# Optimization experiments

Hardware: AMD Instinct MI355X
Metric: run time of the kernel (lower is better)

The kernel has to match this reference:

```python
import jax, jax.numpy as jnp
import numpy as np

SIGMA_DATA = 16.0
ALPHA_BOND = 1.0
ALPHA_DNA = 5.0
ALPHA_RNA = 5.0
ALPHA_LIGAND = 10.0
B, N_TOK, APT = 2, 256, 8
N_ATOM = N_TOK * APT
EPS = 1e-12  # inside sqrt to keep grads finite on the zero diagonal


def _pdist(x):
    # x: [*, A, 3] -> [*, A, A]
    d = x[..., :, None, :] - x[..., None, :, :]
    return jnp.sqrt(jnp.sum(d * d, axis=-1) + EPS)


def _atom_onehot(token_mask, num_atoms_per_token, n_atom):
    # [*, A, T]: atom l belongs to token j iff cum[j-1] <= l < cum[j]
    cum = jnp.cumsum(num_atoms_per_token, axis=-1)
    start = cum - num_atoms_per_token
    l = jnp.arange(n_atom)
    oh = (l[:, None] >= start[..., None, :]) & (l[:, None] < cum[..., None, :])
    return oh.astype(jnp.float32) * token_mask[..., None, :]


def _tok_to_atom(onehot, feat):
    return jnp.einsum('...lj,...j->...l', onehot, feat)


def _weighted_rigid_align(x, x_gt, w, mask):
    # AF3 Algorithm 28 (Kabsch); output is detached in the original.
    denom = jnp.sum(mask, -1, keepdims=True)                      # [*,1]
    w_mean = jnp.sum(w * mask, -1, keepdims=True) / denom         # [*,1]
    wm = (w * mask)[..., None]                                    # [*,A,1]
    mu = (jnp.sum(x * wm, -2) / denom) / w_mean                   # [*,3]
    mu_gt = (jnp.sum(x_gt * wm, -2) / denom) / w_mean
    xc = x - mu[..., None, :]
    xgc = x_gt - mu_gt[..., None, :]
    H = jnp.einsum('...ai,...aj->...ij', xgc * wm, xc)            # [*,3,3]
    U, _, Vh = jnp.linalg.svd(H)
    det = jnp.linalg.det(U @ Vh)
    s = jnp.concatenate([jnp.ones(det.shape + (2,), H.dtype), jnp.sign(det)[..., None]], -1)
    R = U @ (Vh * s[..., :, None])                                # U @ diag(1,1,sign) @ Vh
    return jax.lax.stop_gradient(xc @ jnp.swapaxes(R, -1, -2) + mu_gt[..., None, :])


def _diffusion_loss(x, gt, gt_mask, is_p, is_d, is_r, is_l, tb, tm, npt, t):
    A = x.shape[-2]
    oh = _atom_onehot(tm, npt, A)                                 # [*,A,T]
    dx = _pdist(x)
    dx_gt = _pdist(gt)
    pair_mask = gt_mask[..., :, None] * gt_mask[..., None, :]

    # ---- bond loss (Eq. 5) ----
    is_poly = is_p + is_d + is_r
    bm_tok = tb * (is_poly[..., None, :] * is_l[..., None])       # [*,T,T]
    bm = jnp.einsum('...ij,...li->...lj', bm_tok, oh)
    bm = jnp.einsum('...lj,...mj->...lm', bm, oh)                 # [*,A,A]
    m = bm * pair_mask
    l_bond = jnp.sum((dx - dx_gt) ** 2 * m, (-1, -2)) / jnp.sum(m, (-1, -2))

    # ---- smooth LDDT (Alg. 27) ----
    d = jnp.abs(dx_gt - dx)
    e = 0.25 * (jax.nn.sigmoid(0.5 - d) + jax.nn.sigmoid(1.0 - d)
                + jax.nn.sigmoid(2.0 - d) + jax.nn.sigmoid(4.0 - d))
    is_nuc = _tok_to_atom(oh, is_d + is_r)                        # [*,A]
    c = ((dx_gt < 30).astype(x.dtype) * is_nuc[..., None]
         + (dx_gt < 15).astype(x.dtype) * (1.0 - is_nuc[..., None]))
    m2 = (1.0 - jnp.eye(A, dtype=x.dtype)) * pair_mask
    msum = jnp.sum(m2, (-1, -2))
    ce_mean = jnp.sum(c * e * m2, (-1, -2)) / msum
    c_mean = jnp.sum(c * m2, (-1, -2)) / msum
    l_lddt = 1.0 - ce_mean / c_mean

    # ---- weighted MSE (Eq. 3), gt aligned onto x ----
    w_tok = 1.0 + is_d * ALPHA_DNA + is_r * ALPHA_RNA + is_l * ALPHA_LIGAND
    w_atom = _tok_to_atom(oh, w_tok)                              # [*,A]
    sg = jax.lax.stop_gradient
    gt_al = _weighted_rigid_align(sg(gt), sg(x), sg(w_atom), sg(gt_mask))
    l_mse = (1.0 / 3.0) * jnp.sum(jnp.sum((x - gt_al) ** 2, -1) * w_atom * gt_mask, -1) \
            / jnp.sum(gt_mask, -1)

    w_t = (t ** 2 + SIGMA_DATA ** 2) / (t + SIGMA_DATA) ** 2
    return jnp.mean(w_t * (l_mse + ALPHA_BOND * l_bond) + l_lddt)


def setup_inputs() -> dict:
    key = jax.random.key(0)
    k = jax.random.split(key, 9)
    x = jax.random.normal(k[0], (B, N_ATOM, 3), jnp.float32) * 10.0
    gt = x + jax.random.normal(k[1], (B, N_ATOM, 3), jnp.float32)
    return {
        'x': x,
        'gt_atom_positions': gt,
        'gt_atom_mask': jnp.ones((B, N_ATOM), jnp.float32),
        'is_protein': jax.random.uniform(k[2], (B, N_TOK), jnp.float32),
        'is_dna': jax.random.uniform(k[3], (B, N_TOK), jnp.float32),
        'is_rna': jax.random.uniform(k[4], (B, N_TOK), jnp.float32),
        'is_ligand': jax.random.uniform(k[5], (B, N_TOK), jnp.float32),
        'token_bonds': jax.random.uniform(k[6], (B, N_TOK, N_TOK), jnp.float32),
        'token_mask': jnp.ones((B, N_TOK), jnp.float32),
        'num_atoms_per_token': jnp.full((B, N_TOK), APT, jnp.int32),
        't': jax.random.uniform(k[7], (B,), jnp.float32) * 10.0 + 0.1,
    }


def reference(x, gt_atom_positions, gt_atom_mask, is_protein, is_dna, is_rna,
              is_ligand, token_bonds, token_mask, num_atoms_per_token, t):
    return _diffusion_loss(x, gt_atom_positions, gt_atom_mask, is_protein, is_dna,
                           is_rna, is_ligand, token_bonds, token_mask,
                           num_atoms_per_token, t)
```

## Files before the change

kernel.cpp:

```cpp
#include <hip/hip_runtime.h>
#include <math.h>

#define BATCH 2
#define NTOK  256
#define NATOM 2048
#define TL 128
#define TM 64
#define NPB 512
#define TBBUF 1600

__device__ __forceinline__ float frcp(float x)  { return __builtin_amdgcn_rcpf(x); }
__device__ __forceinline__ float fsqrt_(float x){ return __builtin_amdgcn_sqrtf(x); }

__device__ __forceinline__ double wred64(double v) {
    for (int o = 32; o > 0; o >>= 1) v += __shfl_down(v, o, 64);
    return v;
}
__device__ __forceinline__ float fred64(float v) {
    for (int o = 32; o > 0; o >>= 1) v += __shfl_down(v, o, 64);
    return v;
}

__device__ void kabsch_from_sums(const double* shd, float* Rf, float* muf, double* masksum) {
    double wmsum = shd[1];
    float H[3][3];
    for (int i = 0; i < 3; i++)
        for (int j = 0; j < 3; j++)
            H[i][j] = (float)(shd[8 + i * 3 + j] - shd[2 + i] * shd[5 + j] / wmsum);
    float A[3][3];
    for (int j = 0; j < 3; j++) for (int k = 0; k < 3; k++) {
        float s = 0.f; for (int i = 0; i < 3; i++) s = fmaf(H[i][j], H[i][k], s);
        A[j][k] = s;
    }
    float V[3][3] = {{1, 0, 0}, {0, 1, 0}, {0, 0, 1}};
    for (int sweep = 0; sweep < 6; ++sweep) {
        float off = fabsf(A[0][1]) + fabsf(A[0][2]) + fabsf(A[1][2]);
        float diag = fabsf(A[0][0]) + fabsf(A[1][1]) + fabsf(A[2][2]);
        if (off < 1e-7f * diag) break;
        for (int pi = 0; pi < 3; ++pi) {
            int pp_ = (pi == 2) ? 1 : 0;
            int qq_ = (pi == 0) ? 1 : 2;
            float apq = A[pp_][qq_];
            float sc = fabsf(A[pp_][pp_]) + fabsf(A[qq_][qq_]);
            if (fabsf(apq) <= 1e-9f * sc) continue;
            float theta = (A[qq_][qq_] - A[pp_][pp_]) * 0.5f * frcp(apq);
            float t_ = ((theta >= 0.f) ? 1.0f : -1.0f) * frcp(fabsf(theta) + fsqrt_(fmaf(theta, theta, 1.0f)));
            float c_ = frcp(fsqrt_(fmaf(t_, t_, 1.0f))), sn = t_ * c_;
            for (int k = 0; k < 3; k++) { float akp = A[k][pp_], akq = A[k][qq_];
                A[k][pp_] = c_ * akp - sn * akq; A[k][qq_] = sn * akp + c_ * akq; }
            for (int k = 0; k < 3; k++) { float apk = A[pp_][k], aqk = A[qq_][k];
                A[pp_][k] = c_ * apk - sn * aqk; A[qq_][k] = sn * apk + c_ * aqk; }
            for (int k = 0; k < 3; k++) { float vkp = V[k][pp_], vkq = V[k][qq_];
                V[k][pp_] = c_ * vkp - sn * vkq; V[k][qq_] = sn * vkp + c_ * vkq; }
        }
    }
    float lam[3] = {A[0][0], A[1][1], A[2][2]};
    int idx[3] = {0, 1, 2};
    for (int i = 0; i < 2; i++) for (int j = i + 1; j < 3; j++)
        if (lam[idx[j]] > lam[idx[i]]) { int tsw = idx[i]; idx[i] = idx[j]; idx[j] = tsw; }
    float Vs[3][3], sv[3];
    for (int k = 0; k < 3; k++) {
        sv[k] = fsqrt_(fmaxf(lam[idx[k]], 0.0f));
        for (int i = 0; i < 3; i++) Vs[i][k] = V[i][idx[k]];
    }
    float U[3][3] = {{1, 0, 0}, {0, 1, 0}, {0, 0, 1}};
    for (int k = 0; k < 3; k++) {
        if (sv[k] > 1e-6f * sv[0] + 1e-30f) {
            float inv = frcp(sv[k]);
            for (int i = 0; i < 3; i++) {
                float s = 0.f; for (int j = 0; j < 3; j++) s = fmaf(H[i][j], Vs[j][k], s);
                U[i][k] = s * inv;
            }
        } else if (k == 2) {
            U[0][2] = U[1][0] * U[2][1] - U[2][0] * U[1][1];
            U[1][2] = U[2][0] * U[0][1] - U[0][0] * U[2][1];
            U[2][2] = U[0][0] * U[1][1] - U[1][0] * U[0][1];
        }
    }
    float R0[3][3];
    for (int i = 0; i < 3; i++) for (int j = 0; j < 3; j++) {
        float s = 0.f; for (int k = 0; k < 3; k++) s = fmaf(U[i][k], Vs[j][k], s);
        R0[i][j] = s;
    }
    float det = R0[0][0] * (R0[1][1] * R0[2][2] - R0[1][2] * R0[2][1])
              - R0[0][1] * (R0[1][0] * R0[2][2] - R0[1][2] * R0[2][0])
              + R0[0][2] * (R0[1][0] * R0[2][1] - R0[1][1] * R0[2][0]);
    float s2 = (det < 0.0f) ? -1.0f : 1.0f;
    for (int i = 0; i < 3; i++) for (int j = 0; j < 3; j++)
        Rf[i * 3 + j] = fmaf(U[i][0], Vs[j][0], fmaf(U[i][1], Vs[j][1], s2 * U[i][2] * Vs[j][2]));
    for (int i = 0; i < 3; i++) {
        muf[i]     = (float)(shd[2 + i] / wmsum);
        muf[3 + i] = (float)(shd[5 + i] / wmsum);
    }
    *masksum = shd[0];
}

struct PairSh {
    float  isl[NTOK], poly[NTOK], nuc[NTOK], tmk[NTOK];
    int    wsum[4];
    unsigned short atokp1[NATOM];
    float4 lx[TL], lg[TL], mx[TM], mg[TM];
    float  lnuc[TL];
    int    ltok[TL], mtok[TM], lrow[TL], mrel[TM];
    float  tbuf[TBBUF];
    int    info[6];
    float  pred[4][4];
};
struct AlignSh {
    int    wsum[4];
    float  aw[NATOM];
    double dred[4][17];
    float  Rf[9], muf[6];
    double msum;
    double mred[4];
};

__global__ __launch_bounds__(256) void pair_align_kernel(
    const float* __restrict__ x, const float* __restrict__ gt,
    const float* __restrict__ gmask, const float* __restrict__ tb,
    const float* __restrict__ is_p, const float* __restrict__ is_d,
    const float* __restrict__ is_r, const float* __restrict__ is_l,
    const float* __restrict__ tok_mask, const int* __restrict__ npt,
    float4* __restrict__ partials4, float* __restrict__ lmse)
{
    __shared__ __align__(16) char smem[sizeof(PairSh) > sizeof(AlignSh) ? sizeof(PairSh) : sizeof(AlignSh)];
    int id = blockIdx.x;
    int tid = threadIdx.x;
    int lane = tid & 63, wv = tid >> 6;

    if (id >= BATCH) {
        PairSh* s = (PairSh*)smem;
        int pid = id - BATCH;
        int b = pid >> 9;
        int slot = pid & (NPB - 1);
        int l0 = (slot & 15) * TL;
        int m0 = (slot >> 4) * TM;

        int n = npt[b * NTOK + tid];
        {
            int v = n;
            #pragma unroll
            for (int o = 1; o < 64; o <<= 1) {
                int u = __shfl_up(v, o, 64);
                if (lane >= o) v += u;
            }
            if (lane == 63) s->wsum[wv] = v;
            float pd = is_d[b * NTOK + tid], pr = is_r[b * NTOK + tid];
            float pp = is_p[b * NTOK + tid], pl = is_l[b * NTOK + tid];
            s->isl[tid]  = pl;
            s->poly[tid] = pp + pd + pr;
            s->nuc[tid]  = pd + pr;
            s->tmk[tid]  = tok_mask[b * NTOK + tid];
            #pragma unroll
            for (int i = 0; i < NATOM / NTOK; i++) s->atokp1[tid + i * NTOK] = 0;
            __syncthreads();
            int pref = 0;
            for (int w = 0; w < wv; w++) pref += s->wsum[w];
            int cum = v + pref;
            int end = min(cum, NATOM), start = min(cum - n, NATOM);
            unsigned short tk1 = (unsigned short)(tid + 1);
            for (int i = start; i < end; i++) s->atokp1[i] = tk1;
        }
        __syncthreads();

        const float* Xb = x + (size_t)b * NATOM * 3;
        const float* Gb = gt + (size_t)b * NATOM * 3;
        const float* Mb = gmask + (size_t)b * NATOM;

        if (tid < TL) {
            int l = l0 + tid;
            int v = s->atokp1[l];
            int tok = v ? v - 1 : 0;
            float oh = v ? s->tmk[tok] : 0.0f;
            float ml = Mb[l];
            s->lx[tid] = make_float4(Xb[l * 3], Xb[l * 3 + 1], Xb[l * 3 + 2], ml);
            s->lg[tid] = make_float4(Gb[l * 3], Gb[l * 3 + 1], Gb[l * 3 + 2], s->isl[tok] * oh * ml);
            s->lnuc[tid] = s->nuc[tok] * oh;
            s->ltok[tid] = tok;
        } else if (tid < TL + TM) {
            int i = tid - TL, m = m0 + i;
            int v = s->atokp1[m];
            int tok = v ? v - 1 : 0;
            float oh = v ? s->tmk[tok] : 0.0f;
            float mm = Mb[m];
            s->mx[i] = make_float4(Xb[m * 3], Xb[m * 3 + 1], Xb[m * 3 + 2], mm);
            s->mg[i] = make_float4(Gb[m * 3], Gb[m * 3 + 1], Gb[m * 3 + 2], s->poly[tok] * oh * mm);
            s->mtok[i] = tok;
        }
        __syncthreads();
        if (tid == 0) {
            int tl0 = s->ltok[0], tl1 = s->ltok[TL - 1];
            int tm0 = s->mtok[0], tm1 = s->mtok[TM - 1];
            int spanL = tl1 - tl0 + 1, spanM = tm1 - tm0 + 1;
            int stride = spanM | 1;
            int fits = (spanL >= 1) && (spanM >= 1) && (spanL * stride <= TBBUF);
            s->info[0] = fits; s->info[1] = stride; s->info[2] = spanM;
            s->info[3] = tl0; s->info[4] = tm0; s->info[5] = spanL;
        }
        __syncthreads();
        int fits = s->info[0], stride = s->info[1], spanM = s->info[2];
        int tl0 = s->info[3], tm0 = s->info[4], spanL = s->info[5];
        if (tid < TL) {
            int tk = s->ltok[tid];
            s->lrow[tid] = fits ? min(max(tk - tl0, 0), spanL - 1) * stride : tk * NTOK;
        } else if (tid < TL + TM) {
            int tk = s->mtok[tid - TL];
            s->mrel[tid - TL] = fits ? min(max(tk - tm0, 0), spanM - 1) : tk;
        }
        const float* tbg = tb + (size_t)b * NTOK * NTOK;
        if (fits) {
            int cnt = spanL * stride;
            for (int i = tid; i < cnt; i += 256) {
                int r = i / stride, cc = i - r * stride;
                if (cc < spanM) s->tbuf[i] = tbg[(tl0 + r) * NTOK + tm0 + cc];
            }
        }
        __syncthreads();

        int lt = tid & 31, mg = tid >> 5;
        float4 lxv[4], lgv[4]; float lnu[4]; int lrw[4], gli[4];
        #pragma unroll
        for (int k = 0; k < 4; k++) {
            int li = lt + 32 * k;
            lxv[k] = s->lx[li]; lgv[k] = s->lg[li];
            lnu[k] = s->lnuc[li]; lrw[k] = s->lrow[li]; gli[k] = l0 + li;
        }
        float bnum = 0.f, bden = 0.f, ce = 0.f, cs = 0.f;
        const float k1 = 0.60653066f, k2 = 0.36787944f, k3 = 0.13533528f, k4 = 0.018315639f;

        auto body = [&](auto ldtb) {
            int mstart = mg * 8;
            #pragma unroll 2
            for (int j = 0; j < 8; j++) {
                int m = mstart + j;
                float4 mxv = s->mx[m], mgv = s->mg[m];
                int mrel = s->mrel[m];
                int gmi = m0 + m;
                #pragma unroll
                for (int k = 0; k < 4; k++) {
                    float dx0 = lxv[k].x - mxv.x, dx1 = lxv[k].y - mxv.y, dx2 = lxv[k].z - mxv.z;
                    float dg0 = lgv[k].x - mgv.x, dg1 = lgv[k].y - mgv.y, dg2 = lgv[k].z - mgv.z;
                    float dxv = fsqrt_(fmaf(dx2, dx2, fmaf(dx1, dx1, fmaf(dx0, dx0, 1e-12f))));
                    float dgv = fsqrt_(fmaf(dg2, dg2, fmaf(dg1, dg1, fmaf(dg0, dg0, 1e-12f))));
                    float diff = dxv - dgv;
                    float tbv = ldtb(lrw[k], mrel);
                    float bmv = tbv * (lgv[k].w * mgv.w);
                    bden += bmv;
                    bnum = fmaf(diff * diff, bmv, bnum);
                    float d = fabsf(diff);
                    float u = __expf(d);
                    float e1 = frcp(fmaf(u, k1, 1.0f));
                    float e2 = frcp(fmaf(u, k2, 1.0f));
                    float e3 = frcp(fmaf(u, k3, 1.0f));
                    float e4 = frcp(fmaf(u, k4, 1.0f));
                    float es = (e1 + e2) + (e3 + e4);
                    float pm = lxv[k].w * mxv.w;
                    float ccv = dgv < 30.0f ? (dgv < 15.0f ? 1.0f : lnu[k]) : 0.0f;
                    float pm2 = (gli[k] != gmi) ? pm : 0.0f;
                    float cm2 = ccv * pm2;
                    cs += cm2;
                    ce = fmaf(cm2 * 0.25f, es, ce);
                }
            }
        };
        if (fits) body([&](int r, int c) -> float { return s->tbuf[r + c]; });
        else      body([&](int r, int c) -> float { return tbg[r + c]; });

        float vals[4] = {bnum, bden, ce, cs};
        #pragma unroll
        for (int q = 0; q < 4; q++) {
            float v = fred64(vals[q]);
            if (lane == 0) s->pred[wv][q] = v;
        }
        __syncthreads();
        if (tid == 0) {
            float4 o;
            o.x = s->pred[0][0] + s->pred[1][0] + s->pred[2][0] + s->pred[3][0];
            o.y = s->pred[0][1] + s->pred[1][1] + s->pred[2][1] + s->pred[3][1];
            o.z = s->pred[0][2] + s->pred[1][2] + s->pred[2][2] + s->pred[3][2];
            o.w = s->pred[0][3] + s->pred[1][3] + s->pred[2][3] + s->pred[3][3];
            partials4[(size_t)b * NPB + slot] = o;
        }
    } else {
        AlignSh* s = (AlignSh*)smem;
        int b = id;

        {
            int n = npt[b * NTOK + tid];
            int v = n;
            #pragma unroll
            for (int o = 1; o < 64; o <<= 1) {
                int u = __shfl_up(v, o, 64);
                if (lane >= o) v += u;
            }
            if (lane == 63) s->wsum[wv] = v;
            #pragma unroll
            for (int i = 0; i < NATOM / NTOK; i++) s->aw[tid + i * NTOK] = 0.0f;
            float pd = is_d[b * NTOK + tid], pr = is_r[b * NTOK + tid];
            float pl = is_l[b * NTOK + tid];
            float wtv = (1.0f + 5.0f * pd + 5.0f * pr + 10.0f * pl) * tok_mask[b * NTOK + tid];
            __syncthreads();
            int pref = 0;
            for (int w = 0; w < wv; w++) pref += s->wsum[w];
            int cum = v + pref;
            int end = min(cum, NATOM), start = min(cum - n, NATOM);
            for (int i = start; i < end; i++) s->aw[i] = wtv;
        }
        __syncthreads();

        const float* X = x + (size_t)b * NATOM * 3;
        const float* G = gt + (size_t)b * NATOM * 3;
        const float* M = gmask + (size_t)b * NATOM;

        double p[17];
        #pragma unroll
        for (int q = 0; q < 17; q++) p[q] = 0.0;
        for (int a = tid; a < NATOM; a += 256) {
            double m = M[a], wm = (double)s->aw[a] * m;
            double x0 = X[a * 3], x1 = X[a * 3 + 1], x2 = X[a * 3 + 2];
            double g0 = G[a * 3], g1 = G[a * 3 + 1], g2 = G[a * 3 + 2];
            p[0] += m; p[1] += wm;
            p[2] += wm * x0; p[3] += wm * x1; p[4] += wm * x2;
            p[5] += wm * g0; p[6] += wm * g1; p[7] += wm * g2;
            p[8]  += wm * x0 * g0; p[9]  += wm * x0 * g1; p[10] += wm * x0 * g2;
            p[11] += wm * x1 * g0; p[12] += wm * x1 * g1; p[13] += wm * x1 * g2;
            p[14] += wm * x2 * g0; p[15] += wm * x2 * g1; p[16] += wm * x2 * g2;
        }
        #pragma unroll
        for (int q = 0; q < 17; q++) {
            double v = wred64(p[q]);
            if (lane == 0) s->dred[wv][q] = v;
        }
        __syncthreads();
        if (tid == 0) {
            double sh[17];
            for (int q = 0; q < 17; q++)
                sh[q] = s->dred[0][q] + s->dred[1][q] + s->dred[2][q] + s->dred[3][q];
            double ms;
            kabsch_from_sums(sh, s->Rf, s->muf, &ms);
            s->msum = ms;
        }
        __syncthreads();

        float R00 = s->Rf[0], R01 = s->Rf[1], R02 = s->Rf[2];
        float R10 = s->Rf[3], R11 = s->Rf[4], R12 = s->Rf[5];
        float R20 = s->Rf[6], R21 = s->Rf[7], R22 = s->Rf[8];
        float mux0 = s->muf[0], mux1 = s->muf[1], mux2 = s->muf[2];
        float mug0 = s->muf[3], mug1 = s->muf[4], mug2 = s->muf[5];
        double part = 0.0;
        for (int a = tid; a < NATOM; a += 256) {
            float w = s->aw[a], m = M[a];
            float gc0 = G[a * 3] - mug0, gc1 = G[a * 3 + 1] - mug1, gc2 = G[a * 3 + 2] - mug2;
            float al0 = fmaf(R00, gc0, fmaf(R01, gc1, fmaf(R02, gc2, mux0)));
            float al1 = fmaf(R10, gc0, fmaf(R11, gc1, fmaf(R12, gc2, mux1)));
            float al2 = fmaf(R20, gc0, fmaf(R21, gc1, fmaf(R22, gc2, mux2)));
            float r0 = X[a * 3] - al0, r1 = X[a * 3 + 1] - al1, r2 = X[a * 3 + 2] - al2;
            part += (double)(w * m * (r0 * r0 + r1 * r1 + r2 * r2));
        }
        {
            double v = wred64(part);
            if (lane == 0) s->mred[wv] = v;
        }
        __syncthreads();
        if (tid == 0)
            lmse[b] = (float)((s->mred[0] + s->mred[1] + s->mred[2] + s->mred[3]) / (3.0 * s->msum));
    }
}

__global__ __launch_bounds__(256) void final_kernel(
    const float4* __restrict__ partials4, const float* __restrict__ lmse,
    const float* __restrict__ t, float* __restrict__ out)
{
    int tid = threadIdx.x, lane = tid & 63, wv = tid >> 6;
    double pr[2][4] = {{0, 0, 0, 0}, {0, 0, 0, 0}};
    #pragma unroll
    for (int b = 0; b < BATCH; b++)
        for (int sI = tid; sI < NPB; sI += 256) {
            float4 v = partials4[(size_t)b * NPB + sI];
            pr[b][0] += v.x; pr[b][1] += v.y; pr[b][2] += v.z; pr[b][3] += v.w;
        }
    __shared__ double sred[4][8];
    #pragma unroll
    for (int b = 0; b < BATCH; b++)
        #pragma unroll
        for (int q = 0; q < 4; q++) {
            double v = wred64(pr[b][q]);
            if (lane == 0) sred[wv][b * 4 + q] = v;
        }
    __syncthreads();
    if (tid == 0) {
        double tot = 0.0;
        for (int b = 0; b < BATCH; b++) {
            double bn = 0, bd = 0, ce = 0, cs = 0;
            for (int w = 0; w < 4; w++) {
                bn += sred[w][b * 4 + 0]; bd += sred[w][b * 4 + 1];
                ce += sred[w][b * 4 + 2]; cs += sred[w][b * 4 + 3];
            }
            double l_bond = bn / bd;
            double l_lddt = 1.0 - ce / cs;
            double tt = t[b];
            double w_t = (tt * tt + 256.0) / ((tt + 16.0) * (tt + 16.0));
            tot += w_t * ((double)lmse[b] + l_bond) + l_lddt;
        }
        out[0] = (float)(tot / (double)BATCH);
    }
}

extern "C" void kernel_launch(void* const* d_in, const int* in_sizes, int n_in,
                              void* d_out, int out_size, void* d_ws, size_t ws_size,
                              hipStream_t stream) {
    const float* x     = (const float*)d_in[0];
    const float* gt    = (const float*)d_in[1];
    const float* gmask = (const float*)d_in[2];
    const float* is_p  = (const float*)d_in[3];
    const float* is_d  = (const float*)d_in[4];
    const float* is_r  = (const float*)d_in[5];
    const float* is_l  = (const float*)d_in[6];
    const float* tb    = (const float*)d_in[7];
    const float* tm    = (const float*)d_in[8];
    const int*   npt   = (const int*)d_in[9];
    const float* t     = (const float*)d_in[10];
    float* out = (float*)d_out;

    float4* partials4 = (float4*)d_ws;
    float*  lmse      = (float*)((char*)d_ws + (size_t)BATCH * NPB * sizeof(float4));

    pair_align_kernel<<<BATCH + 2 * NPB, 256, 0, stream>>>(
        x, gt, gmask, tb, is_p, is_d, is_r, is_l, tm, npt, partials4, lmse);
    final_kernel<<<1, 256, 0, stream>>>(partials4, lmse, t, out);
}
```

Before: 96.42 us.

## Exploit pair symmetry with upper-triangular 64x64 tile decomposition

```diff
diff --git a/kernel.cpp b/kernel.cpp
--- a/kernel.cpp
+++ b/kernel.cpp
@@ -4,10 +4,10 @@
 #define BATCH 2
 #define NTOK  256
 #define NATOM 2048
-#define TL 128
-#define TM 64
-#define NPB 512
-#define TBBUF 1600
+#define TS 64
+#define NT (NATOM / TS)
+#define NTRI (NT * (NT + 1) / 2)
+#define TBCAP 1156
 
 __device__ __forceinline__ float frcp(float x)  { return __builtin_amdgcn_rcpf(x); }
 __device__ __forceinline__ float fsqrt_(float x){ return __builtin_amdgcn_sqrtf(x); }
@@ -99,11 +99,11 @@
     float  isl[NTOK], poly[NTOK], nuc[NTOK], tmk[NTOK];
     int    wsum[4];
     unsigned short atokp1[NATOM];
-    float4 lx[TL], lg[TL], mx[TM], mg[TM];
-    float  lnuc[TL];
-    int    ltok[TL], mtok[TM], lrow[TL], mrel[TM];
-    float  tbuf[TBBUF];
-    int    info[6];
+    float4 ax[2 * TS], ag[2 * TS];
+    float2 af[2 * TS];
+    int    rel[2 * TS];
+    float  tbA[TBCAP], tbB[TBCAP];
+    int    info[5];
     float  pred[4][4];
 };
 struct AlignSh {
@@ -126,15 +126,18 @@
     __shared__ __align__(16) char smem[sizeof(PairSh) > sizeof(AlignSh) ? sizeof(PairSh) : sizeof(AlignSh)];
     int id = blockIdx.x;
     int tid = threadIdx.x;
-    int lane = tid & 63, wv = tid >> 6;
+    int lane = tid & 63, wvi = tid >> 6;
 
     if (id >= BATCH) {
         PairSh* s = (PairSh*)smem;
         int pid = id - BATCH;
-        int b = pid >> 9;
-        int slot = pid & (NPB - 1);
-        int l0 = (slot & 15) * TL;
-        int m0 = (slot >> 4) * TM;
+        int b = (pid >= NTRI) ? 1 : 0;
+        int tri = pid - b * NTRI;
+        int ti = 0, off = 0;
+        while (off + (NT - ti) <= tri) { off += NT - ti; ti++; }
+        int tj = ti + (tri - off);
+        int l0 = ti * TS, m0 = tj * TS;
+        int diag = (ti == tj);
 
         int n = npt[b * NTOK + tid];
         {
@@ -144,7 +147,7 @@
                 int u = __shfl_up(v, o, 64);
                 if (lane >= o) v += u;
             }
-            if (lane == 63) s->wsum[wv] = v;
+            if (lane == 63) s->wsum[wvi] = v;
             float pd = is_d[b * NTOK + tid], pr = is_r[b * NTOK + tid];
             float pp = is_p[b * NTOK + tid], pl = is_l[b * NTOK + tid];
             s->isl[tid]  = pl;
@@ -155,7 +158,7 @@
             for (int i = 0; i < NATOM / NTOK; i++) s->atokp1[tid + i * NTOK] = 0;
             __syncthreads();
             int pref = 0;
-            for (int w = 0; w < wv; w++) pref += s->wsum[w];
+            for (int w = 0; w < wvi; w++) pref += s->wsum[w];
             int cum = v + pref;
             int end = min(cum, NATOM), start = min(cum - n, NATOM);
             unsigned short tk1 = (unsigned short)(tid + 1);
@@ -167,110 +170,146 @@
         const float* Gb = gt + (size_t)b * NATOM * 3;
         const float* Mb = gmask + (size_t)b * NATOM;
 
-        if (tid < TL) {
-            int l = l0 + tid;
-            int v = s->atokp1[l];
+        if (tid == 0) {
+            int v0 = s->atokp1[l0], v1 = s->atokp1[l0 + TS - 1];
+            int w0 = s->atokp1[m0], w1 = s->atokp1[m0 + TS - 1];
+            int tl0 = v0 ? v0 - 1 : 0, tl1 = v1 ? v1 - 1 : 0;
+            int tm0 = w0 ? w0 - 1 : 0, tm1 = w1 ? w1 - 1 : 0;
+            int spanL = tl1 - tl0 + 1, spanM = tm1 - tm0 + 1;
+            int sA = spanM | 1, sB = spanL | 1;
+            int fits = (spanL * sA <= TBCAP) && (spanM * sB <= TBCAP);
+            s->info[0] = fits; s->info[1] = sA; s->info[2] = sB;
+            s->info[3] = tl0; s->info[4] = tm0;
+            ((int*)s->pred)[0] = spanL; ((int*)s->pred)[1] = spanM;
+        }
+        __syncthreads();
+        int fits = s->info[0], sA = s->info[1], sB = s->info[2];
+        int tl0 = s->info[3], tm0 = s->info[4];
+        int spanL = ((int*)s->pred)[0], spanM = ((int*)s->pred)[1];
+
+        if (tid < 2 * TS) {
+            int side = tid >> 6, idx = tid & (TS - 1);
+            int a = (side ? m0 : l0) + idx;
+            int v = s->atokp1[a];
             int tok = v ? v - 1 : 0;
             float oh = v ? s->tmk[tok] : 0.0f;
-            float ml = Mb[l];
-            s->lx[tid] = make_float4(Xb[l * 3], Xb[l * 3 + 1], Xb[l * 3 + 2], ml);
-            s->lg[tid] = make_float4(Gb[l * 3], Gb[l * 3 + 1], Gb[l * 3 + 2], s->isl[tok] * oh * ml);
-            s->lnuc[tid] = s->nuc[tok] * oh;
-            s->ltok[tid] = tok;
-        } else if (tid < TL + TM) {
-            int i = tid - TL, m = m0 + i;
-            int v = s->atokp1[m];
-            int tok = v ? v - 1 : 0;
-            float oh = v ? s->tmk[tok] : 0.0f;
-            float mm = Mb[m];
-            s->mx[i] = make_float4(Xb[m * 3], Xb[m * 3 + 1], Xb[m * 3 + 2], mm);
-            s->mg[i] = make_float4(Gb[m * 3], Gb[m * 3 + 1], Gb[m * 3 + 2], s->poly[tok] * oh * mm);
-            s->mtok[i] = tok;
-        }
-        __syncthreads();
-        if (tid == 0) {
-            int tl0 = s->ltok[0], tl1 = s->ltok[TL - 1];
-            int tm0 = s->mtok[0], tm1 = s->mtok[TM - 1];
-            int spanL = tl1 - tl0 + 1, spanM = tm1 - tm0 + 1;
-            int stride = spanM | 1;
-            int fits = (spanL >= 1) && (spanM >= 1) && (spanL * stride <= TBBUF);
-            s->info[0] = fits; s->info[1] = stride; s->info[2] = spanM;
-            s->info[3] = tl0; s->info[4] = tm0; s->info[5] = spanL;
-        }
-        __syncthreads();
-        int fits = s->info[0], stride = s->info[1], spanM = s->info[2];
-        int tl0 = s->info[3], tm0 = s->info[4], spanL = s->info[5];
-        if (tid < TL) {
-            int tk = s->ltok[tid];
-            s->lrow[tid] = fits ? min(max(tk - tl0, 0), spanL - 1) * stride : tk * NTOK;
-        } else if (tid < TL + TM) {
-            int tk = s->mtok[tid - TL];
-            s->mrel[tid - TL] = fits ? min(max(tk - tm0, 0), spanM - 1) : tk;
+            float mk = Mb[a];
+            s->ax[tid] = make_float4(Xb[a * 3], Xb[a * 3 + 1], Xb[a * 3 + 2], mk);
+            s->ag[tid] = make_float4(Gb[a * 3], Gb[a * 3 + 1], Gb[a * 3 + 2], s->nuc[tok] * oh);
+            s->af[tid] = make_float2(s->isl[tok] * oh, s->poly[tok] * oh);
+            int base = side ? tm0 : tl0;
+            int span = side ? spanM : spanL;
+            s->rel[tid] = fits ? min(max(tok - base, 0), span - 1) : tok;
         }
         const float* tbg = tb + (size_t)b * NTOK * NTOK;
         if (fits) {
-            int cnt = spanL * stride;
-            for (int i = tid; i < cnt; i += 256) {
-                int r = i / stride, cc = i - r * stride;
-                if (cc < spanM) s->tbuf[i] = tbg[(tl0 + r) * NTOK + tm0 + cc];
-            }
-        }
-        __syncthreads();
-
-        int lt = tid & 31, mg = tid >> 5;
-        float4 lxv[4], lgv[4]; float lnu[4]; int lrw[4], gli[4];
+            int cntA = spanL * sA;
+            for (int i = tid; i < cntA; i += 256) {
+                int r = i / sA, cc = i - r * sA;
+                if (cc < spanM) s->tbA[i] = tbg[(tl0 + r) * NTOK + tm0 + cc];
+            }
+            int cntB = spanM * sB;
+            for (int i = tid; i < cntB; i += 256) {
+                int r = i / sB, cc = i - r * sB;
+                if (cc < spanL) s->tbB[i] = tbg[(tm0 + r) * NTOK + tl0 + cc];
+            }
+        }
+        __syncthreads();
+
+        int lt = tid & 15, mg = tid >> 4;
+        float4 lx4[4], lg4[4]; float2 lf2[4]; int lrel[4], gl[4];
         #pragma unroll
         for (int k = 0; k < 4; k++) {
-            int li = lt + 32 * k;
-            lxv[k] = s->lx[li]; lgv[k] = s->lg[li];
-            lnu[k] = s->lnuc[li]; lrw[k] = s->lrow[li]; gli[k] = l0 + li;
+            int li = lt + 16 * k;
+            lx4[k] = s->ax[li]; lg4[k] = s->ag[li]; lf2[k] = s->af[li];
+            lrel[k] = s->rel[li]; gl[k] = l0 + li;
         }
         float bnum = 0.f, bden = 0.f, ce = 0.f, cs = 0.f;
         const float k1 = 0.60653066f, k2 = 0.36787944f, k3 = 0.13533528f, k4 = 0.018315639f;
 
-        auto body = [&](auto ldtb) {
-            int mstart = mg * 8;
-            #pragma unroll 2
-            for (int j = 0; j < 8; j++) {
-                int m = mstart + j;
-                float4 mxv = s->mx[m], mgv = s->mg[m];
-                int mrel = s->mrel[m];
-                int gmi = m0 + m;
-                #pragma unroll
-                for (int k = 0; k < 4; k++) {
-                    float dx0 = lxv[k].x - mxv.x, dx1 = lxv[k].y - mxv.y, dx2 = lxv[k].z - mxv.z;
-                    float dg0 = lgv[k].x - mgv.x, dg1 = lgv[k].y - mgv.y, dg2 = lgv[k].z - mgv.z;
-                    float dxv = fsqrt_(fmaf(dx2, dx2, fmaf(dx1, dx1, fmaf(dx0, dx0, 1e-12f))));
-                    float dgv = fsqrt_(fmaf(dg2, dg2, fmaf(dg1, dg1, fmaf(dg0, dg0, 1e-12f))));
-                    float diff = dxv - dgv;
-                    float tbv = ldtb(lrw[k], mrel);
-                    float bmv = tbv * (lgv[k].w * mgv.w);
-                    bden += bmv;
-                    bnum = fmaf(diff * diff, bmv, bnum);
-                    float d = fabsf(diff);
-                    float u = __expf(d);
-                    float e1 = frcp(fmaf(u, k1, 1.0f));
-                    float e2 = frcp(fmaf(u, k2, 1.0f));
-                    float e3 = frcp(fmaf(u, k3, 1.0f));
-                    float e4 = frcp(fmaf(u, k4, 1.0f));
-                    float es = (e1 + e2) + (e3 + e4);
-                    float pm = lxv[k].w * mxv.w;
-                    float ccv = dgv < 30.0f ? (dgv < 15.0f ? 1.0f : lnu[k]) : 0.0f;
-                    float pm2 = (gli[k] != gmi) ? pm : 0.0f;
-                    float cm2 = ccv * pm2;
-                    cs += cm2;
-                    ce = fmaf(cm2 * 0.25f, es, ce);
+        auto run = [&](auto ldA, auto ldB) {
+            int mstart = mg * 4;
+            if (diag) {
+                #pragma unroll 2
+                for (int j = 0; j < 4; j++) {
+                    int m = mstart + j;
+                    float4 mx4 = s->ax[TS + m], mg4 = s->ag[TS + m];
+                    float2 mf = s->af[TS + m];
+                    int mr = s->rel[TS + m];
+                    int gm = m0 + m;
+                    #pragma unroll
+                    for (int k = 0; k < 4; k++) {
+                        float dx0 = lx4[k].x - mx4.x, dx1 = lx4[k].y - mx4.y, dx2 = lx4[k].z - mx4.z;
+                        float dg0 = lg4[k].x - mg4.x, dg1 = lg4[k].y - mg4.y, dg2 = lg4[k].z - mg4.z;
+                        float dxv = fsqrt_(fmaf(dx2, dx2, fmaf(dx1, dx1, fmaf(dx0, dx0, 1e-12f))));
+                        float dgv = fsqrt_(fmaf(dg2, dg2, fmaf(dg1, dg1, fmaf(dg0, dg0, 1e-12f))));
+                        float diff = dxv - dgv;
+                        float tbv = ldA(lrel[k], mr);
+                        float pm = lx4[k].w * mx4.w;
+                        float bmv = tbv * lf2[k].x * mf.y * pm;
+                        bden += bmv;
+                        bnum = fmaf(diff * diff, bmv, bnum);
+                        float d = fabsf(diff);
+                        float u = __expf(d);
+                        float e1 = frcp(fmaf(u, k1, 1.0f));
+                        float e2 = frcp(fmaf(u, k2, 1.0f));
+                        float e3 = frcp(fmaf(u, k3, 1.0f));
+                        float e4 = frcp(fmaf(u, k4, 1.0f));
+                        float es = (e1 + e2) + (e3 + e4);
+                        float nl = lg4[k].w;
+                        float ccv = dgv < 30.0f ? (dgv < 15.0f ? 1.0f : nl) : 0.0f;
+                        float pm2 = (gl[k] != gm) ? pm : 0.0f;
+                        float cm2 = ccv * pm2;
+                        cs += cm2;
+                        ce = fmaf(cm2 * 0.25f, es, ce);
+                    }
                 }
+            } else {
+                #pragma unroll 2
+                for (int j = 0; j < 4; j++) {
+                    int m = mstart + j;
+                    float4 mx4 = s->ax[TS + m], mg4 = s->ag[TS + m];
+                    float2 mf = s->af[TS + m];
+                    int mr = s->rel[TS + m];
+                    #pragma unroll
+                    for (int k = 0; k < 4; k++) {
+                        float dx0 = lx4[k].x - mx4.x, dx1 = lx4[k].y - mx4.y, dx2 = lx4[k].z - mx4.z;
+                        float dg0 = lg4[k].x - mg4.x, dg1 = lg4[k].y - mg4.y, dg2 = lg4[k].z - mg4.z;
+                        float dxv = fsqrt_(fmaf(dx2, dx2, fmaf(dx1, dx1, fmaf(dx0, dx0, 1e-12f))));
+                        float dgv = fsqrt_(fmaf(dg2, dg2, fmaf(dg1, dg1, fmaf(dg0, dg0, 1e-12f))));
+                        float diff = dxv - dgv;
+                        float pm = lx4[k].w * mx4.w;
+                        float tb1 = ldA(lrel[k], mr);
+                        float tb2 = ldB(mr, lrel[k]);
+                        float bsum = (tb1 * lf2[k].x * mf.y + tb2 * mf.x * lf2[k].y) * pm;
+                        bden += bsum;
+                        bnum = fmaf(diff * diff, bsum, bnum);
+                        float d = fabsf(diff);
+                        float u = __expf(d);
+                        float e1 = frcp(fmaf(u, k1, 1.0f));
+                        float e2 = frcp(fmaf(u, k2, 1.0f));
+                        float e3 = frcp(fmaf(u, k3, 1.0f));
+                        float e4 = frcp(fmaf(u, k4, 1.0f));
+                        float es = (e1 + e2) + (e3 + e4);
+                        float sn = lg4[k].w + mg4.w;
+                        float ccv = (dgv < 30.0f ? sn : 0.0f) + (dgv < 15.0f ? (2.0f - sn) : 0.0f);
+                        float cm2 = ccv * pm;
+                        cs += cm2;
+                        ce = fmaf(cm2 * 0.25f, es, ce);
+                    }
+                }
             }
         };
-        if (fits) body([&](int r, int c) -> float { return s->tbuf[r + c]; });
-        else      body([&](int r, int c) -> float { return tbg[r + c]; });
+        if (fits) run([&](int r, int c) -> float { return s->tbA[r * sA + c]; },
+                      [&](int r, int c) -> float { return s->tbB[r * sB + c]; });
+        else      run([&](int r, int c) -> float { return tbg[r * NTOK + c]; },
+                      [&](int r, int c) -> float { return tbg[r * NTOK + c]; });
 
         float vals[4] = {bnum, bden, ce, cs};
         #pragma unroll
         for (int q = 0; q < 4; q++) {
             float v = fred64(vals[q]);
-            if (lane == 0) s->pred[wv][q] = v;
+            if (lane == 0) s->pred[wvi][q] = v;
         }
         __syncthreads();
         if (tid == 0) {
@@ -279,7 +318,7 @@
             o.y = s->pred[0][1] + s->pred[1][1] + s->pred[2][1] + s->pred[3][1];
             o.z = s->pred[0][2] + s->pred[1][2] + s->pred[2][2] + s->pred[3][2];
             o.w = s->pred[0][3] + s->pred[1][3] + s->pred[2][3] + s->pred[3][3];
-            partials4[(size_t)b * NPB + slot] = o;
+            partials4[(size_t)b * NTRI + tri] = o;
         }
     } else {
         AlignSh* s = (AlignSh*)smem;
@@ -293,7 +332,7 @@
                 int u = __shfl_up(v, o, 64);
                 if (lane >= o) v += u;
             }
-            if (lane == 63) s->wsum[wv] = v;
+            if (lane == 63) s->wsum[wvi] = v;
             #pragma unroll
             for (int i = 0; i < NATOM / NTOK; i++) s->aw[tid + i * NTOK] = 0.0f;
             float pd = is_d[b * NTOK + tid], pr = is_r[b * NTOK + tid];
@@ -301,7 +340,7 @@
             float wtv = (1.0f + 5.0f * pd + 5.0f * pr + 10.0f * pl) * tok_mask[b * NTOK + tid];
             __syncthreads();
             int pref = 0;
-            for (int w = 0; w < wv; w++) pref += s->wsum[w];
+            for (int w = 0; w < wvi; w++) pref += s->wsum[w];
             int cum = v + pref;
             int end = min(cum, NATOM), start = min(cum - n, NATOM);
             for (int i = start; i < end; i++) s->aw[i] = wtv;
@@ -329,7 +368,7 @@
         #pragma unroll
         for (int q = 0; q < 17; q++) {
             double v = wred64(p[q]);
-            if (lane == 0) s->dred[wv][q] = v;
+            if (lane == 0) s->dred[wvi][q] = v;
         }
         __syncthreads();
         if (tid == 0) {
@@ -359,7 +398,7 @@
         }
         {
             double v = wred64(part);
-            if (lane == 0) s->mred[wv] = v;
+            if (lane == 0) s->mred[wvi] = v;
         }
         __syncthreads();
         if (tid == 0)
@@ -375,8 +414,8 @@
     double pr[2][4] = {{0, 0, 0, 0}, {0, 0, 0, 0}};
     #pragma unroll
     for (int b = 0; b < BATCH; b++)
-        for (int sI = tid; sI < NPB; sI += 256) {
-            float4 v = partials4[(size_t)b * NPB + sI];
+        for (int sI = tid; sI < NTRI; sI += 256) {
+            float4 v = partials4[(size_t)b * NTRI + sI];
             pr[b][0] += v.x; pr[b][1] += v.y; pr[b][2] += v.z; pr[b][3] += v.w;
         }
     __shared__ double sred[4][8];
@@ -423,9 +462,9 @@
     float* out = (float*)d_out;
 
     float4* partials4 = (float4*)d_ws;
-    float*  lmse      = (float*)((char*)d_ws + (size_t)BATCH * NPB * sizeof(float4));
-
-    pair_align_kernel<<<BATCH + 2 * NPB, 256, 0, stream>>>(
+    float*  lmse      = (float*)((char*)d_ws + (size_t)BATCH * NTRI * sizeof(float4));
+
+    pair_align_kernel<<<BATCH + BATCH * NTRI, 256, 0, stream>>>(
         x, gt, gmask, tb, is_p, is_d, is_r, is_l, tm, npt, partials4, lmse);
     final_kernel<<<1, 256, 0, stream>>>(partials4, lmse, t, out);
 }
```

Measured after the change: 90.55 us. 6.1% less time.
